# Performance work log

Measured on AMD Instinct MI355X. Metric: run time of the kernel, lower is better.

The kernel has to match this reference:

```python
import jax, jax.numpy as jnp
import numpy as np

BETA = 5.5
ALPHA = 0.5

def _l2norm(x, eps=1e-12):
    # matches torch F.normalize(dim=-1): x / max(||x||, eps)
    n = jnp.sqrt(jnp.sum(x * x, axis=-1, keepdims=True))
    return x / jnp.maximum(n, eps)

def setup_inputs() -> dict:
    key = jax.random.key(0)
    k1, k2 = jax.random.split(key)
    query_features = jax.random.normal(k1, (4096, 512), dtype=jnp.float32)
    support_keys = jax.random.normal(k2, (16384, 512), dtype=jnp.float32)
    return {"query_features": query_features, "support_keys": support_keys}

def reference(query_features, support_keys):
    cache_keys = _l2norm(support_keys)              # (N, D)
    q = _l2norm(query_features)                     # (B, D)
    affinity = jnp.einsum('bd,nd->bn', q, cache_keys)   # (B, N) cosine sims
    affinity = jnp.exp(-BETA * (1.0 - affinity))
    retrieved = jnp.einsum('bn,nd->bd', affinity, cache_keys)  # (B, D)
    return query_features + ALPHA * retrieved
```

## Files before the change

### kernel.cpp

```cpp
#include <hip/hip_runtime.h>
#include <cstdint>
#include <cstddef>

#define BETA 5.5f
#define ALPHA 0.5f

constexpr int D   = 512;
constexpr int NB  = 4096;
constexpr int NK  = 16384;
constexpr int BQ  = 64;
constexpr int BN  = 64;
constexpr int NSPLIT = 4;
constexpr int NRANGE = NK / NSPLIT;
constexpr int CHUNKS = NRANGE / BN;
constexpr int KROW = D + 8;
constexpr int PROW = BN + 8;

typedef __attribute__((ext_vector_type(8)))  short    short8;
typedef __attribute__((ext_vector_type(4)))  float    floatx4;
typedef __attribute__((ext_vector_type(4)))  uint32_t uint4v;
typedef __attribute__((ext_vector_type(2)))  uint32_t uint2v;

__device__ inline uint32_t f2bf1(float f) {
  union { float f; uint32_t u; } v; v.f = f;
  return (v.u + 0x7FFFu + ((v.u >> 16) & 1u)) >> 16;
}
__device__ inline uint32_t pack2(float a, float b) {
  return f2bf1(a) | (f2bf1(b) << 16);
}

__device__ inline void load_lds16(const void* g, void* l) {
  __builtin_amdgcn_global_load_lds(
      (const __attribute__((address_space(1))) uint32_t*)g,
      (__attribute__((address_space(3))) uint32_t*)l, 16, 0, 0);
}

__global__ void norm_q_kernel(const float* __restrict__ q,
                              float* __restrict__ out,
                              unsigned short* __restrict__ Qn) {
  const int wave = threadIdx.x >> 6, lane = threadIdx.x & 63;
  const int row = blockIdx.x * 4 + wave;
  const float4* qr = (const float4*)(q + (size_t)row * D);
  float4 a = qr[lane * 2];
  float4 b = qr[lane * 2 + 1];
  float ss = a.x*a.x + a.y*a.y + a.z*a.z + a.w*a.w
           + b.x*b.x + b.y*b.y + b.z*b.z + b.w*b.w;
#pragma unroll
  for (int m = 32; m >= 1; m >>= 1) ss += __shfl_xor(ss, m, 64);
  const float sc = 1.0f / fmaxf(sqrtf(ss), 1e-12f);
  float4* orow = (float4*)(out + (size_t)row * D);
  orow[lane * 2]     = a;
  orow[lane * 2 + 1] = b;
  uint4v w;
  w.x = pack2(a.x*sc, a.y*sc); w.y = pack2(a.z*sc, a.w*sc);
  w.z = pack2(b.x*sc, b.y*sc); w.w = pack2(b.z*sc, b.w*sc);
  *(uint4v*)(Qn + (size_t)row * D + lane * 8) = w;
}

__global__ void norm_k_kernel(const float* __restrict__ k,
                              unsigned short* __restrict__ Kn,
                              unsigned short* __restrict__ KnT) {
  __shared__ unsigned short tile[64 * KROW];
  const int wave = threadIdx.x >> 6, lane = threadIdx.x & 63;
  const int n0 = blockIdx.x * 64;
#pragma unroll
  for (int i = 0; i < 4; ++i) {
    const int rl = wave * 4 + i;
    const int n  = n0 + rl;
    const float4* kr = (const float4*)(k + (size_t)n * D);
    float4 a = kr[lane * 2], b = kr[lane * 2 + 1];
    float ss = a.x*a.x + a.y*a.y + a.z*a.z + a.w*a.w
             + b.x*b.x + b.y*b.y + b.z*b.z + b.w*b.w;
#pragma unroll
    for (int m = 32; m >= 1; m >>= 1) ss += __shfl_xor(ss, m, 64);
    const float sc = 1.0f / fmaxf(sqrtf(ss), 1e-12f);
    uint4v w;
    w.x = pack2(a.x*sc, a.y*sc); w.y = pack2(a.z*sc, a.w*sc);
    w.z = pack2(b.x*sc, b.y*sc); w.w = pack2(b.z*sc, b.w*sc);
    *(uint4v*)(Kn + (size_t)n * D + lane * 8) = w;
    *(uint4v*)&tile[rl * KROW + lane * 8]     = w;
  }
  __syncthreads();
  const int dsub = threadIdx.x >> 3;
  const int nl   = (threadIdx.x & 7) * 8;
#pragma unroll
  for (int iter = 0; iter < 4; ++iter) {
    const int d = iter * 128 + dsub;
    uint4v w;
    w.x = (uint32_t)tile[(nl+0)*KROW + d] | ((uint32_t)tile[(nl+1)*KROW + d] << 16);
    w.y = (uint32_t)tile[(nl+2)*KROW + d] | ((uint32_t)tile[(nl+3)*KROW + d] << 16);
    w.z = (uint32_t)tile[(nl+4)*KROW + d] | ((uint32_t)tile[(nl+5)*KROW + d] << 16);
    w.w = (uint32_t)tile[(nl+6)*KROW + d] | ((uint32_t)tile[(nl+7)*KROW + d] << 16);
    *(uint4v*)(KnT + (size_t)d * NK + n0 + nl) = w;
  }
}

__global__ __launch_bounds__(512, 2) void fused_kernel(
    const unsigned short* __restrict__ Qn,
    const unsigned short* __restrict__ Kn,
    const unsigned short* __restrict__ KnT,
    float* __restrict__ out) {
  __shared__ unsigned short K_lds[2][BN * KROW];
  __shared__ unsigned short P_lds[2][BQ * PROW];

  const int tid  = threadIdx.x;
  const int wave = tid >> 6, lane = tid & 63;
  const int l15  = lane & 15, quad = lane >> 4;
  const int nsplit = blockIdx.x & (NSPLIT - 1);
  const int qtile  = blockIdx.x >> 2;
  const int q0     = qtile * BQ;
  const int nbase  = nsplit * NRANGE;

  auto stage = [&](int ch, int buf) {
#pragma unroll
    for (int i = 0; i < 8; ++i) {
      const int row = wave * 8 + i;
      load_lds16(Kn + (size_t)(nbase + ch * BN + row) * D + lane * 8,
                 &K_lds[buf][row * KROW]);
    }
  };

  if (wave < 4) {
    const int qh = wave & 1, nh = wave >> 1;
    short8 qf[2][16];
    {
      const unsigned short* qrow0 = Qn + (size_t)(q0 + qh * 32 + l15) * D + quad * 8;
#pragma unroll
      for (int qt = 0; qt < 2; ++qt)
#pragma unroll
        for (int kb = 0; kb < 16; ++kb)
          qf[qt][kb] = *(const short8*)(qrow0 + (size_t)qt * 16 * D + kb * 32);
    }

    auto gemm1x = [&](int buf, int pbuf) {
      floatx4 sacc[2][2] = {};
#pragma unroll
      for (int kb = 0; kb < 16; ++kb) {
        short8 a0 = *(const short8*)&K_lds[buf][(nh*32 +      l15) * KROW + kb*32 + quad*8];
        short8 a1 = *(const short8*)&K_lds[buf][(nh*32 + 16 + l15) * KROW + kb*32 + quad*8];
        sacc[0][0] = __builtin_amdgcn_mfma_f32_16x16x32_bf16(a0, qf[0][kb], sacc[0][0], 0, 0, 0);
        sacc[0][1] = __builtin_amdgcn_mfma_f32_16x16x32_bf16(a0, qf[1][kb], sacc[0][1], 0, 0, 0);
        sacc[1][0] = __builtin_amdgcn_mfma_f32_16x16x32_bf16(a1, qf[0][kb], sacc[1][0], 0, 0, 0);
        sacc[1][1] = __builtin_amdgcn_mfma_f32_16x16x32_bf16(a1, qf[1][kb], sacc[1][1], 0, 0, 0);
      }
#pragma unroll
      for (int qt = 0; qt < 2; ++qt)
#pragma unroll
        for (int nt = 0; nt < 2; ++nt) {
          const floatx4 s = sacc[nt][qt];
          uint2v w;
          w.x = pack2(__expf(BETA * (s[0] - 1.f)), __expf(BETA * (s[1] - 1.f)));
          w.y = pack2(__expf(BETA * (s[2] - 1.f)), __expf(BETA * (s[3] - 1.f)));
          *(uint2v*)&P_lds[pbuf][(qh*32 + qt*16 + l15) * PROW + nh*32 + nt*16 + quad*4] = w;
        }
    };

    stage(0, 0);
    __syncthreads();
    stage(1, 1);
    gemm1x(0, 0);
    __syncthreads();

#pragma unroll 1
    for (int c = 0; c + 2 < CHUNKS; ++c) {
      const int cur = c & 1, nxt = cur ^ 1;
      stage(c + 2, cur);
      gemm1x(nxt, nxt);
      __syncthreads();
    }
    gemm1x((CHUNKS - 1) & 1, (CHUNKS - 1) & 1);
    __syncthreads();
  } else {
    const int w4 = wave - 4;
    floatx4 oacc[4][8] = {};
    short8 ktf[2][8];
    const unsigned short* ktbase = KnT + (size_t)(w4 * 128 + l15) * NK + nbase + quad * 8;

    auto ktf_half = [&](int ch, int kb2) {
#pragma unroll
      for (int td = 0; td < 8; ++td)
        ktf[kb2][td] = *(const short8*)(ktbase + (size_t)td * 16 * NK + ch * BN + kb2 * 32);
    };
    auto gemm2_half = [&](int pbuf, int kb2) {
      short8 pf[4];
#pragma unroll
      for (int tr = 0; tr < 4; ++tr)
        pf[tr] = *(const short8*)&P_lds[pbuf][(tr*16 + l15) * PROW + kb2*32 + quad*8];
#pragma unroll
      for (int td = 0; td < 8; ++td)
#pragma unroll
        for (int tr = 0; tr < 4; ++tr)
          oacc[tr][td] = __builtin_amdgcn_mfma_f32_16x16x32_bf16(
              pf[tr], ktf[kb2][td], oacc[tr][td], 0, 0, 0);
    };

    stage(0, 0);
    __syncthreads();
    stage(1, 1);
    ktf_half(0, 0); ktf_half(0, 1);
    __syncthreads();

#pragma unroll 1
    for (int c = 0; c + 2 < CHUNKS; ++c) {
      const int cur = c & 1;
      stage(c + 2, cur);
      gemm2_half(cur, 0);
      ktf_half(c + 1, 0);
      gemm2_half(cur, 1);
      ktf_half(c + 1, 1);
      __syncthreads();
    }
    {
      const int cur = (CHUNKS - 2) & 1;
      gemm2_half(cur, 0); ktf_half(CHUNKS - 1, 0);
      gemm2_half(cur, 1); ktf_half(CHUNKS - 1, 1);
      __syncthreads();
    }
    {
      const int cur = (CHUNKS - 1) & 1;
      gemm2_half(cur, 0);
      gemm2_half(cur, 1);
    }

    const int colbase = w4 * 128 + l15;
#pragma unroll
    for (int tr = 0; tr < 4; ++tr)
#pragma unroll
      for (int td = 0; td < 8; ++td)
#pragma unroll
        for (int r = 0; r < 4; ++r)
          atomicAdd(out + (size_t)(q0 + tr*16 + quad*4 + r) * D + colbase + td*16,
                    ALPHA * oacc[tr][td][r]);
  }
}

extern "C" void kernel_launch(void* const* d_in, const int* in_sizes, int n_in,
                              void* d_out, int out_size, void* d_ws, size_t ws_size,
                              hipStream_t stream) {
  (void)in_sizes; (void)n_in; (void)out_size; (void)ws_size;
  const float* q = (const float*)d_in[0];
  const float* k = (const float*)d_in[1];
  float* out = (float*)d_out;
  unsigned short* Qn  = (unsigned short*)d_ws;
  unsigned short* Kn  = Qn + (size_t)NB * D;
  unsigned short* KnT = Kn + (size_t)NK * D;

  hipLaunchKernelGGL(norm_q_kernel, dim3(NB / 4),  dim3(256),  0, stream, q, out, Qn);
  hipLaunchKernelGGL(norm_k_kernel, dim3(NK / 64), dim3(1024), 0, stream, k, Kn, KnT);
  hipLaunchKernelGGL(fused_kernel, dim3((NB / BQ) * NSPLIT), dim3(512), 0, stream,
                     Qn, Kn, KnT, out);
}
```

Baseline: 322.8 us.

## Load K fragments directly into registers and drop LDS staging of K

The four score-producing waves no longer stage 64-row K chunks into a double-buffered LDS tile. Each wave instead loads its bf16 K fragments from global memory straight into registers, in a four-stage software pipeline across the d-dimension groups. This removes the roughly 130 KB K buffer from shared memory, which should allow more resident blocks per CU, and trims the block-wide waits on async LDS loads. The __syncthreads calls become a lighter barrier that waits only on LDS counters, and s_setprio is raised around the MFMA bursts. The trade-off is redundant global and L1 traffic for K across waves, plus higher register pressure.

```diff
diff --git a/kernel.cpp b/kernel.cpp
--- a/kernel.cpp
+++ b/kernel.cpp
@@ -29,10 +29,8 @@
   return f2bf1(a) | (f2bf1(b) << 16);
 }
 
-__device__ inline void load_lds16(const void* g, void* l) {
-  __builtin_amdgcn_global_load_lds(
-      (const __attribute__((address_space(1))) uint32_t*)g,
-      (__attribute__((address_space(3))) uint32_t*)l, 16, 0, 0);
+__device__ inline void region_barrier() {
+  asm volatile("s_waitcnt lgkmcnt(0)\n\ts_barrier" ::: "memory");
 }
 
 __global__ void norm_q_kernel(const float* __restrict__ q,
@@ -100,7 +98,6 @@
     const unsigned short* __restrict__ Kn,
     const unsigned short* __restrict__ KnT,
     float* __restrict__ out) {
-  __shared__ unsigned short K_lds[2][BN * KROW];
   __shared__ unsigned short P_lds[2][BQ * PROW];
 
   const int tid  = threadIdx.x;
@@ -111,15 +108,6 @@
   const int q0     = qtile * BQ;
   const int nbase  = nsplit * NRANGE;
 
-  auto stage = [&](int ch, int buf) {
-#pragma unroll
-    for (int i = 0; i < 8; ++i) {
-      const int row = wave * 8 + i;
-      load_lds16(Kn + (size_t)(nbase + ch * BN + row) * D + lane * 8,
-                 &K_lds[buf][row * KROW]);
-    }
-  };
-
   if (wave < 4) {
     const int qh = wave & 1, nh = wave >> 1;
     short8 qf[2][16];
@@ -132,17 +120,48 @@
           qf[qt][kb] = *(const short8*)(qrow0 + (size_t)qt * 16 * D + kb * 32);
     }
 
-    auto gemm1x = [&](int buf, int pbuf) {
-      floatx4 sacc[2][2] = {};
-#pragma unroll
-      for (int kb = 0; kb < 16; ++kb) {
-        short8 a0 = *(const short8*)&K_lds[buf][(nh*32 +      l15) * KROW + kb*32 + quad*8];
-        short8 a1 = *(const short8*)&K_lds[buf][(nh*32 + 16 + l15) * KROW + kb*32 + quad*8];
-        sacc[0][0] = __builtin_amdgcn_mfma_f32_16x16x32_bf16(a0, qf[0][kb], sacc[0][0], 0, 0, 0);
-        sacc[0][1] = __builtin_amdgcn_mfma_f32_16x16x32_bf16(a0, qf[1][kb], sacc[0][1], 0, 0, 0);
-        sacc[1][0] = __builtin_amdgcn_mfma_f32_16x16x32_bf16(a1, qf[0][kb], sacc[1][0], 0, 0, 0);
-        sacc[1][1] = __builtin_amdgcn_mfma_f32_16x16x32_bf16(a1, qf[1][kb], sacc[1][1], 0, 0, 0);
+    const unsigned short* pK0 = Kn + (size_t)(nbase + nh * 32 + l15) * D + quad * 8;
+    const unsigned short* pK1 = pK0 + (size_t)16 * D;
+
+    short8 kfA[8], kfB[8];
+    floatx4 sacc[2][2];
+
+    auto ldK = [&](short8* kf, int c, int g) {
+      const size_t cb = (size_t)c * 64 * D;
+#pragma unroll
+      for (int i = 0; i < 4; ++i) {
+        kf[2*i]   = *(const short8*)(pK0 + cb + (g*4 + i) * 32);
+        kf[2*i+1] = *(const short8*)(pK1 + cb + (g*4 + i) * 32);
       }
+    };
+    auto mfma_g = [&](const short8* kf, int g) {
+      __builtin_amdgcn_s_setprio(1);
+#pragma unroll
+      for (int i = 0; i < 4; ++i) {
+        const int kb = g*4 + i;
+        sacc[0][0] = __builtin_amdgcn_mfma_f32_16x16x32_bf16(kf[2*i],   qf[0][kb], sacc[0][0], 0, 0, 0);
+        sacc[0][1] = __builtin_amdgcn_mfma_f32_16x16x32_bf16(kf[2*i],   qf[1][kb], sacc[0][1], 0, 0, 0);
+        sacc[1][0] = __builtin_amdgcn_mfma_f32_16x16x32_bf16(kf[2*i+1], qf[0][kb], sacc[1][0], 0, 0, 0);
+        sacc[1][1] = __builtin_amdgcn_mfma_f32_16x16x32_bf16(kf[2*i+1], qf[1][kb], sacc[1][1], 0, 0, 0);
+      }
+      __builtin_amdgcn_s_setprio(0);
+    };
+
+    ldK(kfA, 0, 0);
+#pragma unroll 1
+    for (int c = 0; c < CHUNKS; ++c) {
+#pragma unroll
+      for (int nt = 0; nt < 2; ++nt)
+#pragma unroll
+        for (int qt = 0; qt < 2; ++qt) sacc[nt][qt] = (floatx4){0.f, 0.f, 0.f, 0.f};
+
+      ldK(kfB, c, 1);  mfma_g(kfA, 0);
+      ldK(kfA, c, 2);  mfma_g(kfB, 1);
+      ldK(kfB, c, 3);  mfma_g(kfA, 2);
+      if (c + 1 < CHUNKS) ldK(kfA, c + 1, 0);
+      mfma_g(kfB, 3);
+
+      const int pb = c & 1;
 #pragma unroll
       for (int qt = 0; qt < 2; ++qt)
 #pragma unroll
@@ -151,76 +170,50 @@
           uint2v w;
           w.x = pack2(__expf(BETA * (s[0] - 1.f)), __expf(BETA * (s[1] - 1.f)));
           w.y = pack2(__expf(BETA * (s[2] - 1.f)), __expf(BETA * (s[3] - 1.f)));
-          *(uint2v*)&P_lds[pbuf][(qh*32 + qt*16 + l15) * PROW + nh*32 + nt*16 + quad*4] = w;
+          *(uint2v*)&P_lds[pb][(qh*32 + qt*16 + l15) * PROW + nh*32 + nt*16 + quad*4] = w;
         }
-    };
-
-    stage(0, 0);
-    __syncthreads();
-    stage(1, 1);
-    gemm1x(0, 0);
-    __syncthreads();
-
-#pragma unroll 1
-    for (int c = 0; c + 2 < CHUNKS; ++c) {
-      const int cur = c & 1, nxt = cur ^ 1;
-      stage(c + 2, cur);
-      gemm1x(nxt, nxt);
-      __syncthreads();
+      region_barrier();
     }
-    gemm1x((CHUNKS - 1) & 1, (CHUNKS - 1) & 1);
-    __syncthreads();
   } else {
     const int w4 = wave - 4;
     floatx4 oacc[4][8] = {};
-    short8 ktf[2][8];
-    const unsigned short* ktbase = KnT + (size_t)(w4 * 128 + l15) * NK + nbase + quad * 8;
-
-    auto ktf_half = [&](int ch, int kb2) {
+    short8 kt0[8], kt1[8];
+    const unsigned short* ktb = KnT + (size_t)(w4 * 128 + l15) * NK + nbase + quad * 8;
+
+    auto ldKT = [&](short8* kt, int c, int kb2) {
 #pragma unroll
       for (int td = 0; td < 8; ++td)
-        ktf[kb2][td] = *(const short8*)(ktbase + (size_t)td * 16 * NK + ch * BN + kb2 * 32);
-    };
-    auto gemm2_half = [&](int pbuf, int kb2) {
+        kt[td] = *(const short8*)(ktb + (size_t)td * 16 * NK + c * 64 + kb2 * 32);
+    };
+    auto g2 = [&](int pb, int kb2, const short8* kt) {
       short8 pf[4];
 #pragma unroll
       for (int tr = 0; tr < 4; ++tr)
-        pf[tr] = *(const short8*)&P_lds[pbuf][(tr*16 + l15) * PROW + kb2*32 + quad*8];
+        pf[tr] = *(const short8*)&P_lds[pb][(tr*16 + l15) * PROW + kb2*32 + quad*8];
+      __builtin_amdgcn_s_setprio(1);
 #pragma unroll
       for (int td = 0; td < 8; ++td)
 #pragma unroll
         for (int tr = 0; tr < 4; ++tr)
           oacc[tr][td] = __builtin_amdgcn_mfma_f32_16x16x32_bf16(
-              pf[tr], ktf[kb2][td], oacc[tr][td], 0, 0, 0);
-    };
-
-    stage(0, 0);
-    __syncthreads();
-    stage(1, 1);
-    ktf_half(0, 0); ktf_half(0, 1);
-    __syncthreads();
+              pf[tr], kt[td], oacc[tr][td], 0, 0, 0);
+      __builtin_amdgcn_s_setprio(0);
+    };
+
+    ldKT(kt0, 0, 0); ldKT(kt1, 0, 1);
+    region_barrier();
 
 #pragma unroll 1
-    for (int c = 0; c + 2 < CHUNKS; ++c) {
-      const int cur = c & 1;
-      stage(c + 2, cur);
-      gemm2_half(cur, 0);
-      ktf_half(c + 1, 0);
-      gemm2_half(cur, 1);
-      ktf_half(c + 1, 1);
-      __syncthreads();
+    for (int c = 1; c < CHUNKS; ++c) {
+      const int pb = (c - 1) & 1;
+      g2(pb, 0, kt0);
+      ldKT(kt0, c, 0);
+      g2(pb, 1, kt1);
+      ldKT(kt1, c, 1);
+      region_barrier();
     }
-    {
-      const int cur = (CHUNKS - 2) & 1;
-      gemm2_half(cur, 0); ktf_half(CHUNKS - 1, 0);
-      gemm2_half(cur, 1); ktf_half(CHUNKS - 1, 1);
-      __syncthreads();
-    }
-    {
-      const int cur = (CHUNKS - 1) & 1;
-      gemm2_half(cur, 0);
-      gemm2_half(cur, 1);
-    }
+    g2((CHUNKS - 1) & 1, 0, kt0);
+    g2((CHUNKS - 1) & 1, 1, kt1);
 
     const int colbase = w4 * 128 + l15;
 #pragma unroll
@@ -228,9 +221,9 @@
 #pragma unroll
       for (int td = 0; td < 8; ++td)
 #pragma unroll
-        for (int r = 0; r < 4; ++r)
-          atomicAdd(out + (size_t)(q0 + tr*16 + quad*4 + r) * D + colbase + td*16,
-                    ALPHA * oacc[tr][td][r]);
+      for (int r = 0; r < 4; ++r)
+        atomicAdd(out + (size_t)(q0 + tr*16 + quad*4 + r) * D + colbase + td*16,
+                  ALPHA * oacc[tr][td][r]);
   }
 }
 
```

New measurement: 449.4 us. +39.2%, slower.
